# Optimization experiments

Measured on AMD Instinct MI355X. Metric: run time of the kernel, lower is better.

Reference implementation:

```python
import jax, jax.numpy as jnp
import numpy as np

N = 35709   # vertices
F = 70789   # triangles
B = 64
CAMERA_DISTANCE = 10.0
FOCAL = 1015.0
IMAGE_SIZE = 224

SH_A = (np.pi, 2 * np.pi / np.sqrt(3.0), 2 * np.pi / np.sqrt(8.0))
SH_C = (1 / np.sqrt(4 * np.pi), np.sqrt(3.0) / np.sqrt(4 * np.pi), 3 * np.sqrt(5.0) / np.sqrt(12 * np.pi))


def _persc_proj():
    center = IMAGE_SIZE / 2
    m = np.array([FOCAL, 0, center, 0, FOCAL, center, 0, 0, 1], dtype=np.float32).reshape(3, 3).T
    return jnp.asarray(m)


def setup_inputs() -> dict:
    key = jax.random.key(0)
    ks = jax.random.split(key, 9)
    return {
        "coeffs": jax.random.normal(ks[0], (B, 257), jnp.float32),
        "meanshape": jax.random.normal(ks[1], (3 * N,), jnp.float32),
        "idBase": jax.random.normal(ks[2], (3 * N, 80), jnp.float32),
        "exBase": jax.random.normal(ks[3], (3 * N, 64), jnp.float32),
        "meantex": jax.random.uniform(ks[4], (3 * N,), jnp.float32) * 255.0,
        "texBase": jax.random.normal(ks[5], (3 * N, 80), jnp.float32),
        "persc_proj": _persc_proj(),
        "init_lit": jnp.array([0.8, 0, 0, 0, 0, 0, 0, 0, 0], jnp.float32).reshape(1, 1, 9),
        "point_buf": jax.random.randint(ks[6], (N, 8), 0, F + 1),   # index F = zero-pad row
        "face_buf": jax.random.randint(ks[7], (F, 3), 0, N),
        "keypoints": jax.random.randint(ks[8], (68,), 0, N),
    }


def _l2norm(x):
    # matches torch F.normalize(p=2, eps=1e-12)
    return x / jnp.maximum(jnp.linalg.norm(x, axis=-1, keepdims=True), 1e-12)


def _rotation(angles):
    x, y, z = angles[:, 0], angles[:, 1], angles[:, 2]
    o, zr = jnp.ones_like(x), jnp.zeros_like(x)
    cx, sx = jnp.cos(x), jnp.sin(x)
    cy, sy = jnp.cos(y), jnp.sin(y)
    cz, sz = jnp.cos(z), jnp.sin(z)
    rx = jnp.stack([o, zr, zr, zr, cx, -sx, zr, sx, cx], -1).reshape(-1, 3, 3)
    ry = jnp.stack([cy, zr, sy, zr, o, zr, -sy, zr, cy], -1).reshape(-1, 3, 3)
    rz = jnp.stack([cz, -sz, zr, sz, cz, zr, zr, zr, o], -1).reshape(-1, 3, 3)
    return jnp.transpose(rz @ ry @ rx, (0, 2, 1))


def _compute_norm(face_shape, face_buf, point_buf):
    tri = face_shape[:, face_buf]                 # (B, F, 3verts, 3xyz) gather
    e1 = tri[:, :, 0] - tri[:, :, 1]
    e2 = tri[:, :, 1] - tri[:, :, 2]
    fn = _l2norm(jnp.cross(e1, e2))               # (B, F, 3)
    fn = jnp.concatenate([fn, jnp.zeros((fn.shape[0], 1, 3), fn.dtype)], axis=1)
    vn = jnp.sum(fn[:, point_buf], axis=2)        # (B, N, 3) gather-sum over 8 faces
    return _l2norm(vn)


def _compute_color(face_texture, face_norm, gamma, init_lit):
    a, c = SH_A, SH_C
    g = gamma.reshape(gamma.shape[0], 3, 9) + init_lit   # (B, 3, 9)
    g = jnp.transpose(g, (0, 2, 1))                      # (B, 9, 3)
    nx, ny, nz = face_norm[..., 0:1], face_norm[..., 1:2], face_norm[..., 2:3]
    Y = jnp.concatenate([
        a[0] * c[0] * jnp.ones_like(nx),
        -a[1] * c[1] * ny,
        a[1] * c[1] * nz,
        -a[1] * c[1] * nx,
        a[2] * c[2] * nx * ny,
        -a[2] * c[2] * ny * nz,
        0.5 * a[2] * c[2] / np.sqrt(3.0) * (3 * nz ** 2 - 1),
        -a[2] * c[2] * nx * nz,
        0.5 * a[2] * c[2] * (nx ** 2 - ny ** 2)], axis=-1)   # (B, N, 9)
    rgb = jnp.einsum('bnk,bkc->bnc', Y, g)
    return rgb * face_texture


def reference(coeffs, meanshape, idBase, exBase, meantex, texBase, persc_proj, init_lit, point_buf, face_buf, keypoints):
    id_c, ex_c, tex_c = coeffs[:, 0:80], coeffs[:, 80:144], coeffs[:, 144:224]
    angles, gamma, trans = coeffs[:, 224:227], coeffs[:, 227:254], coeffs[:, 254:257]
    Bsz = coeffs.shape[0]
    # shape blending (dense GEMMs)
    shape_flat = (jnp.einsum('ij,aj->ai', idBase, id_c)
                  + jnp.einsum('ij,aj->ai', exBase, ex_c)
                  + meanshape[None])
    face_shape = shape_flat.reshape(Bsz, -1, 3)
    rot = _rotation(angles)
    face_shape_t = face_shape @ rot + trans[:, None, :]
    # to camera: z -> camera_distance - z
    face_vertex = jnp.concatenate([face_shape_t[..., :2], CAMERA_DISTANCE - face_shape_t[..., 2:]], axis=-1)
    # perspective projection
    proj = face_vertex @ persc_proj
    face_proj = proj[..., :2] / proj[..., 2:]
    landmark = face_proj[:, keypoints, :]
    # texture blending
    face_texture = ((jnp.einsum('ij,aj->ai', texBase, tex_c) + meantex[None]) / 255.0).reshape(Bsz, -1, 3)
    # mesh normals on untransformed shape, rotated into camera frame
    face_norm = _compute_norm(face_shape, face_buf, point_buf)
    face_norm_r = face_norm @ rot
    face_color = _compute_color(face_texture, face_norm_r, gamma, init_lit)
    return face_vertex, face_color, landmark
```

## Files before the change

kernel.cpp:

```cpp
#include <hip/hip_runtime.h>

#define N_V 35709
#define N_F 70789
#define NR  (3*N_V)
#define NB  64

#define WS_ROT    0
#define WS_GM     576
#define WS_CTRS   2304
#define WS_CTRT   11520
#define WS_SHAPET 16640

__global__ __launch_bounds__(64) void k_setup_rot(
    const float* __restrict__ coeffs, const float* __restrict__ init_lit,
    float* __restrict__ rotM, float* __restrict__ gm)
{
    int b = threadIdx.x;
    const float* cb = coeffs + b * 257;

    float ax = cb[224], ay = cb[225], az = cb[226];
    float cx = cosf(ax), sx = sinf(ax);
    float cy = cosf(ay), sy = sinf(ay);
    float cz = cosf(az), sz = sinf(az);
    float m[9];
    m[0] = cz * cy;
    m[1] = cz * sy * sx - sz * cx;
    m[2] = sz * sx + cz * sy * cx;
    m[3] = sz * cy;
    m[4] = cz * cx + sz * sy * sx;
    m[5] = sz * sy * cx - cz * sx;
    m[6] = -sy;
    m[7] = cy * sx;
    m[8] = cy * cx;
#pragma unroll
    for (int k = 0; k < 9; k++) rotM[b * 9 + k] = m[k];

#pragma unroll
    for (int k = 0; k < 9; k++) {
        float il = init_lit[k];
#pragma unroll
        for (int c = 0; c < 3; c++)
            gm[b * 27 + k * 3 + c] = cb[227 + c * 9 + k] + il;
    }
}

__global__ __launch_bounds__(64) void k_transpose(
    const float* __restrict__ coeffs,
    float* __restrict__ ctrS, float* __restrict__ ctrT)
{
    int j = blockIdx.x;
    int b = threadIdx.x;
    float v = coeffs[b * 257 + j];
    if (j < 144) ctrS[j * 64 + b] = v;
    else         ctrT[(j - 144) * 64 + b] = v;
}

__global__ __launch_bounds__(256) void k_gemm_tile(
    const float* __restrict__ idBase, const float* __restrict__ exBase,
    const float* __restrict__ texBase, const float* __restrict__ meanshape,
    const float* __restrict__ meantex,
    const float* __restrict__ ctrS, const float* __restrict__ ctrT,
    float* __restrict__ shapeT,
    float* __restrict__ texT,
    float* __restrict__ shape3,
    int write_s3, int tex_transposed)
{
    __shared__ __align__(16) float As[16][68];
    __shared__ __align__(16) float Bs[16][64];

    const int t  = threadIdx.x;
    const int tn = t & 15;
    const int tm = t >> 4;
    const int r0 = blockIdx.x * 64;

    const int srow = t >> 2;
    const int sc   = t & 3;
    int srg = r0 + srow; if (srg > NR - 1) srg = NR - 1;

    float acc[4][4];

#pragma unroll
    for (int i = 0; i < 4; i++)
#pragma unroll
        for (int j = 0; j < 4; j++) acc[i][j] = 0.f;

    for (int kc = 0; kc < 9; kc++) {
        const float* src;
        int ld, k0;
        if (kc < 5) { src = idBase; ld = 80; k0 = kc * 16; }
        else        { src = exBase; ld = 64; k0 = (kc - 5) * 16; }

        {
            float4 v = *(const float4*)(src + (size_t)srg * ld + k0 + sc * 4);
            As[sc * 4 + 0][srow] = v.x;
            As[sc * 4 + 1][srow] = v.y;
            As[sc * 4 + 2][srow] = v.z;
            As[sc * 4 + 3][srow] = v.w;
        }
        ((float4*)&Bs[0][0])[t] = ((const float4*)(ctrS + (size_t)kc * 16 * 64))[t];
        __syncthreads();

#pragma unroll
        for (int k = 0; k < 16; k++) {
            float4 a = *(const float4*)&As[k][tm * 4];
            float4 b = *(const float4*)&Bs[k][tn * 4];
            float av[4] = {a.x, a.y, a.z, a.w};
            float bv[4] = {b.x, b.y, b.z, b.w};
#pragma unroll
            for (int i = 0; i < 4; i++)
#pragma unroll
                for (int j = 0; j < 4; j++)
                    acc[i][j] += av[i] * bv[j];
        }
        __syncthreads();
    }

#pragma unroll
    for (int i = 0; i < 4; i++) {
        int rg = r0 + tm * 4 + i;
        if (rg < NR) {
            float ms = meanshape[rg];
            float s0 = acc[i][0] + ms, s1 = acc[i][1] + ms;
            float s2 = acc[i][2] + ms, s3 = acc[i][3] + ms;
            float4 o = {s0, s1, s2, s3};
            *(float4*)(shapeT + (size_t)rg * 64 + tn * 4) = o;
            if (write_s3) {
                int v = rg / 3;
                int c = rg - v * 3;
                float* p = shape3 + ((size_t)v * 64 + tn * 4) * 3 + c;
                p[0] = s0; p[3] = s1; p[6] = s2; p[9] = s3;
            }
        }
    }

#pragma unroll
    for (int i = 0; i < 4; i++)
#pragma unroll
        for (int j = 0; j < 4; j++) acc[i][j] = 0.f;

    for (int kc = 0; kc < 5; kc++) {
        int k0 = kc * 16;
        {
            float4 v = *(const float4*)(texBase + (size_t)srg * 80 + k0 + sc * 4);
            As[sc * 4 + 0][srow] = v.x;
            As[sc * 4 + 1][srow] = v.y;
            As[sc * 4 + 2][srow] = v.z;
            As[sc * 4 + 3][srow] = v.w;
        }
        ((float4*)&Bs[0][0])[t] = ((const float4*)(ctrT + (size_t)kc * 16 * 64))[t];
        __syncthreads();

#pragma unroll
        for (int k = 0; k < 16; k++) {
            float4 a = *(const float4*)&As[k][tm * 4];
            float4 b = *(const float4*)&Bs[k][tn * 4];
            float av[4] = {a.x, a.y, a.z, a.w};
            float bv[4] = {b.x, b.y, b.z, b.w};
#pragma unroll
            for (int i = 0; i < 4; i++)
#pragma unroll
                for (int j = 0; j < 4; j++)
                    acc[i][j] += av[i] * bv[j];
        }
        __syncthreads();
    }

    const float inv255 = 1.0f / 255.0f;
    if (tex_transposed) {
#pragma unroll
        for (int i = 0; i < 4; i++) {
            int rg = r0 + tm * 4 + i;
            if (rg < NR) {
                float mt = meantex[rg];
                float4 o = {(acc[i][0] + mt) * inv255, (acc[i][1] + mt) * inv255,
                            (acc[i][2] + mt) * inv255, (acc[i][3] + mt) * inv255};
                *(float4*)(texT + (size_t)rg * 64 + tn * 4) = o;
            }
        }
    } else {
#pragma unroll
        for (int i = 0; i < 4; i++) {
            int rg = r0 + tm * 4 + i;
            if (rg < NR) {
                float mt = meantex[rg];
#pragma unroll
                for (int j = 0; j < 4; j++)
                    texT[(size_t)(tn * 4 + j) * NR + rg] = (acc[i][j] + mt) * inv255;
            }
        }
    }
}

__global__ __launch_bounds__(256) void k_facenorm3(
    const float* __restrict__ shape3,
    const int* __restrict__ face_buf,
    float* __restrict__ fnT3)
{
    int wave = threadIdx.x >> 6;
    int b    = threadIdx.x & 63;
    int f0   = blockIdx.x * 32 + wave * 8;
#pragma unroll
    for (int fr = 0; fr < 8; fr++) {
        int f = f0 + fr;
        if (f < N_F) {
            int i0 = face_buf[f * 3 + 0];
            int i1 = face_buf[f * 3 + 1];
            int i2 = face_buf[f * 3 + 2];
            const float* p0 = shape3 + ((size_t)i0 * 64 + b) * 3;
            const float* p1 = shape3 + ((size_t)i1 * 64 + b) * 3;
            const float* p2 = shape3 + ((size_t)i2 * 64 + b) * 3;
            float p0x = p0[0], p0y = p0[1], p0z = p0[2];
            float p1x = p1[0], p1y = p1[1], p1z = p1[2];
            float p2x = p2[0], p2y = p2[1], p2z = p2[2];
            float e1x = p0x - p1x, e1y = p0y - p1y, e1z = p0z - p1z;
            float e2x = p1x - p2x, e2y = p1y - p2y, e2z = p1z - p2z;
            float ccx = e1y * e2z - e1z * e2y;
            float ccy = e1z * e2x - e1x * e2z;
            float ccz = e1x * e2y - e1y * e2x;
            float l = sqrtf(ccx * ccx + ccy * ccy + ccz * ccz);
            float inv = 1.0f / fmaxf(l, 1e-12f);
            float* o = fnT3 + ((size_t)f * 64 + b) * 3;
            o[0] = ccx * inv; o[1] = ccy * inv; o[2] = ccz * inv;
        } else if (f == N_F) {
            float* o = fnT3 + ((size_t)f * 64 + b) * 3;
            o[0] = 0.f; o[1] = 0.f; o[2] = 0.f;
        }
    }
}

__global__ __launch_bounds__(256) void k_facenorm(
    const float* __restrict__ shapeT,
    const int* __restrict__ face_buf,
    float* __restrict__ fnT3)
{
    int wave = threadIdx.x >> 6;
    int b    = threadIdx.x & 63;
    int f0   = blockIdx.x * 32 + wave * 8;
#pragma unroll
    for (int fr = 0; fr < 8; fr++) {
        int f = f0 + fr;
        if (f < N_F) {
            int i0 = face_buf[f * 3 + 0];
            int i1 = face_buf[f * 3 + 1];
            int i2 = face_buf[f * 3 + 2];
            float p0x = shapeT[(size_t)(3 * i0)     * 64 + b];
            float p0y = shapeT[(size_t)(3 * i0 + 1) * 64 + b];
            float p0z = shapeT[(size_t)(3 * i0 + 2) * 64 + b];
            float p1x = shapeT[(size_t)(3 * i1)     * 64 + b];
            float p1y = shapeT[(size_t)(3 * i1 + 1) * 64 + b];
            float p1z = shapeT[(size_t)(3 * i1 + 2) * 64 + b];
            float p2x = shapeT[(size_t)(3 * i2)     * 64 + b];
            float p2y = shapeT[(size_t)(3 * i2 + 1) * 64 + b];
            float p2z = shapeT[(size_t)(3 * i2 + 2) * 64 + b];
            float e1x = p0x - p1x, e1y = p0y - p1y, e1z = p0z - p1z;
            float e2x = p1x - p2x, e2y = p1y - p2y, e2z = p1z - p2z;
            float ccx = e1y * e2z - e1z * e2y;
            float ccy = e1z * e2x - e1x * e2z;
            float ccz = e1x * e2y - e1y * e2x;
            float l = sqrtf(ccx * ccx + ccy * ccy + ccz * ccz);
            float inv = 1.0f / fmaxf(l, 1e-12f);
            float* o = fnT3 + ((size_t)f * 64 + b) * 3;
            o[0] = ccx * inv; o[1] = ccy * inv; o[2] = ccz * inv;
        } else if (f == N_F) {
            float* o = fnT3 + ((size_t)f * 64 + b) * 3;
            o[0] = 0.f; o[1] = 0.f; o[2] = 0.f;
        }
    }
}

__global__ __launch_bounds__(256) void k_vertex_fn(
    const float* __restrict__ shapeT,
    const float* __restrict__ texT,
    const float* __restrict__ fnT3,
    const float* __restrict__ rotM, const float* __restrict__ gm,
    const float* __restrict__ coeffs,
    const int* __restrict__ point_buf,
    float* __restrict__ out_vertex, float* __restrict__ out_color)
{
    __shared__ float sh[64 * 49];
    int wave = threadIdx.x >> 6;
    int b    = threadIdx.x & 63;
    int v0   = blockIdx.x * 16;
    int nvalid = N_V - v0; if (nvalid > 16) nvalid = 16;
    int kmax = 3 * nvalid;

    float m0 = rotM[b * 9 + 0], m1 = rotM[b * 9 + 1], m2 = rotM[b * 9 + 2];
    float m3 = rotM[b * 9 + 3], m4 = rotM[b * 9 + 4], m5 = rotM[b * 9 + 5];
    float m6 = rotM[b * 9 + 6], m7 = rotM[b * 9 + 7], m8 = rotM[b * 9 + 8];
    float tx = coeffs[b * 257 + 254], ty = coeffs[b * 257 + 255], tz = coeffs[b * 257 + 256];
    float g[27];
#pragma unroll
    for (int k = 0; k < 27; k++) g[k] = gm[b * 27 + k];

    const float A0C0 = 0.8862269254527580f;
    const float A1C1 = 1.7724538509055159f;
    const float A2C2 = 2.4270323912f;
    const float C6   = 0.7006239022f;
    const float C8   = 1.2135161956f;

    int pf[4][8];
    float sxv[4], syv[4], szv[4];
    float t0v[4], t1v[4], t2v[4];
#pragma unroll
    for (int vr = 0; vr < 4; vr++) {
        int v = v0 + wave * 4 + vr;
        int vc = (v < N_V) ? v : (N_V - 1);
#pragma unroll
        for (int k = 0; k < 8; k++) pf[vr][k] = point_buf[vc * 8 + k];
        sxv[vr] = shapeT[(size_t)(3 * vc)     * 64 + b];
        syv[vr] = shapeT[(size_t)(3 * vc + 1) * 64 + b];
        szv[vr] = shapeT[(size_t)(3 * vc + 2) * 64 + b];
        t0v[vr] = texT[(size_t)(3 * vc)     * 64 + b];
        t1v[vr] = texT[(size_t)(3 * vc + 1) * 64 + b];
        t2v[vr] = texT[(size_t)(3 * vc + 2) * 64 + b];
    }

    float vert[4][3];
    float col[4][3];

#pragma unroll
    for (int vr = 0; vr < 4; vr++) {
        float fx[8], fy[8], fz[8];
#pragma unroll
        for (int k = 0; k < 8; k++) {
            const float* fp = fnT3 + ((size_t)pf[vr][k] * 64 + b) * 3;
            fx[k] = fp[0]; fy[k] = fp[1]; fz[k] = fp[2];
        }

        float vx = m0 * sxv[vr] + m1 * syv[vr] + m2 * szv[vr] + tx;
        float vy = m3 * sxv[vr] + m4 * syv[vr] + m5 * szv[vr] + ty;
        float vz = m6 * sxv[vr] + m7 * syv[vr] + m8 * szv[vr] + tz;
        vert[vr][0] = vx; vert[vr][1] = vy; vert[vr][2] = 10.0f - vz;

        float nx = 0.f, ny = 0.f, nz = 0.f;
#pragma unroll
        for (int k = 0; k < 8; k++) { nx += fx[k]; ny += fy[k]; nz += fz[k]; }
        float l = sqrtf(nx * nx + ny * ny + nz * nz);
        float inv = 1.0f / fmaxf(l, 1e-12f);
        nx *= inv; ny *= inv; nz *= inv;

        float rx = m0 * nx + m1 * ny + m2 * nz;
        float ry = m3 * nx + m4 * ny + m5 * nz;
        float rz = m6 * nx + m7 * ny + m8 * nz;

        float Y0 = A0C0;
        float Y1 = -A1C1 * ry;
        float Y2 =  A1C1 * rz;
        float Y3 = -A1C1 * rx;
        float Y4 =  A2C2 * rx * ry;
        float Y5 = -A2C2 * ry * rz;
        float Y6 =  C6 * (3.f * rz * rz - 1.f);
        float Y7 = -A2C2 * rx * rz;
        float Y8 =  C8 * (rx * rx - ry * ry);

        float tex3[3] = {t0v[vr], t1v[vr], t2v[vr]};
#pragma unroll
        for (int c = 0; c < 3; c++) {
            float rgb = Y0 * g[0 + c] + Y1 * g[3 + c] + Y2 * g[6 + c] + Y3 * g[9 + c] +
                        Y4 * g[12 + c] + Y5 * g[15 + c] + Y6 * g[18 + c] + Y7 * g[21 + c] +
                        Y8 * g[24 + c];
            col[vr][c] = rgb * tex3[c];
        }
    }

#pragma unroll
    for (int vr = 0; vr < 4; vr++)
#pragma unroll
        for (int c = 0; c < 3; c++)
            sh[b * 49 + (wave * 4 + vr) * 3 + c] = vert[vr][c];
    __syncthreads();
#pragma unroll 4
    for (int it = 0; it < 12; it++) {
        int f = it * 256 + threadIdx.x;
        int bb = f / 48, k = f - bb * 48;
        if (k < kmax)
            __builtin_nontemporal_store(sh[bb * 49 + k],
                                        out_vertex + (size_t)bb * NR + 3 * (size_t)v0 + k);
    }
    __syncthreads();

#pragma unroll
    for (int vr = 0; vr < 4; vr++)
#pragma unroll
        for (int c = 0; c < 3; c++)
            sh[b * 49 + (wave * 4 + vr) * 3 + c] = col[vr][c];
    __syncthreads();
#pragma unroll 4
    for (int it = 0; it < 12; it++) {
        int f = it * 256 + threadIdx.x;
        int bb = f / 48, k = f - bb * 48;
        if (k < kmax)
            __builtin_nontemporal_store(sh[bb * 49 + k],
                                        out_color + (size_t)bb * NR + 3 * (size_t)v0 + k);
    }
}

__global__ __launch_bounds__(256) void k_vertex(
    const float* __restrict__ shapeT,
    const float* __restrict__ texT,
    const float* __restrict__ rotM, const float* __restrict__ gm,
    const float* __restrict__ coeffs,
    const int* __restrict__ point_buf, const int* __restrict__ face_buf,
    float* __restrict__ out_vertex, float* __restrict__ out_color,
    int tex_in_out)
{
    __shared__ float sh[64 * 97];
    int wave = threadIdx.x >> 6;
    int b    = threadIdx.x & 63;
    int v0   = blockIdx.x * 32;
    int nvalid = N_V - v0; if (nvalid > 32) nvalid = 32;
    int kmax = 3 * nvalid;

    float m0 = rotM[b * 9 + 0], m1 = rotM[b * 9 + 1], m2 = rotM[b * 9 + 2];
    float m3 = rotM[b * 9 + 3], m4 = rotM[b * 9 + 4], m5 = rotM[b * 9 + 5];
    float m6 = rotM[b * 9 + 6], m7 = rotM[b * 9 + 7], m8 = rotM[b * 9 + 8];
    float tx = coeffs[b * 257 + 254], ty = coeffs[b * 257 + 255], tz = coeffs[b * 257 + 256];
    float g[27];
#pragma unroll
    for (int k = 0; k < 27; k++) g[k] = gm[b * 27 + k];

    const float A0C0 = 0.8862269254527580f;
    const float A1C1 = 1.7724538509055159f;
    const float A2C2 = 2.4270323912f;
    const float C6   = 0.7006239022f;
    const float C8   = 1.2135161956f;

    float vert[8][3];
    float col[8][3];

#pragma unroll
    for (int vr = 0; vr < 8; vr++) {
        int v = v0 + wave * 8 + vr;
        bool valid = (v < N_V);
        int vc = valid ? v : (N_V - 1);

        float sx0 = shapeT[(size_t)(3 * vc)     * 64 + b];
        float sy0 = shapeT[(size_t)(3 * vc + 1) * 64 + b];
        float sz0 = shapeT[(size_t)(3 * vc + 2) * 64 + b];

        float vx = m0 * sx0 + m1 * sy0 + m2 * sz0 + tx;
        float vy = m3 * sx0 + m4 * sy0 + m5 * sz0 + ty;
        float vz = m6 * sx0 + m7 * sy0 + m8 * sz0 + tz;
        vert[vr][0] = vx; vert[vr][1] = vy; vert[vr][2] = 10.0f - vz;

        float nx = 0.f, ny = 0.f, nz = 0.f;
#pragma unroll
        for (int k = 0; k < 8; k++) {
            int f = point_buf[vc * 8 + k];
            if (f < N_F) {
                int i0 = face_buf[f * 3], i1 = face_buf[f * 3 + 1], i2 = face_buf[f * 3 + 2];
                float p0x = shapeT[(size_t)(3 * i0)     * 64 + b];
                float p0y = shapeT[(size_t)(3 * i0 + 1) * 64 + b];
                float p0z = shapeT[(size_t)(3 * i0 + 2) * 64 + b];
                float p1x = shapeT[(size_t)(3 * i1)     * 64 + b];
                float p1y = shapeT[(size_t)(3 * i1 + 1) * 64 + b];
                float p1z = shapeT[(size_t)(3 * i1 + 2) * 64 + b];
                float p2x = shapeT[(size_t)(3 * i2)     * 64 + b];
                float p2y = shapeT[(size_t)(3 * i2 + 1) * 64 + b];
                float p2z = shapeT[(size_t)(3 * i2 + 2) * 64 + b];
                float e1x = p0x - p1x, e1y = p0y - p1y, e1z = p0z - p1z;
                float e2x = p1x - p2x, e2y = p1y - p2y, e2z = p1z - p2z;
                float ccx = e1y * e2z - e1z * e2y;
                float ccy = e1z * e2x - e1x * e2z;
                float ccz = e1x * e2y - e1y * e2x;
                float l = sqrtf(ccx * ccx + ccy * ccy + ccz * ccz);
                float inv = 1.0f / fmaxf(l, 1e-12f);
                nx += ccx * inv; ny += ccy * inv; nz += ccz * inv;
            }
        }
        float l = sqrtf(nx * nx + ny * ny + nz * nz);
        float inv = 1.0f / fmaxf(l, 1e-12f);
        nx *= inv; ny *= inv; nz *= inv;

        float rx = m0 * nx + m1 * ny + m2 * nz;
        float ry = m3 * nx + m4 * ny + m5 * nz;
        float rz = m6 * nx + m7 * ny + m8 * nz;

        float Y0 = A0C0;
        float Y1 = -A1C1 * ry;
        float Y2 =  A1C1 * rz;
        float Y3 = -A1C1 * rx;
        float Y4 =  A2C2 * rx * ry;
        float Y5 = -A2C2 * ry * rz;
        float Y6 =  C6 * (3.f * rz * rz - 1.f);
        float Y7 = -A2C2 * rx * rz;
        float Y8 =  C8 * (rx * rx - ry * ry);

        float t0, t1, t2;
        if (tex_in_out) {
            size_t ob = (size_t)b * NR + 3 * (size_t)vc;
            t0 = out_color[ob]; t1 = out_color[ob + 1]; t2 = out_color[ob + 2];
        } else {
            t0 = texT[(size_t)(3 * vc)     * 64 + b];
            t1 = texT[(size_t)(3 * vc + 1) * 64 + b];
            t2 = texT[(size_t)(3 * vc + 2) * 64 + b];
        }
        float tex3[3] = {t0, t1, t2};
#pragma unroll
        for (int c = 0; c < 3; c++) {
            float rgb = Y0 * g[0 + c] + Y1 * g[3 + c] + Y2 * g[6 + c] + Y3 * g[9 + c] +
                        Y4 * g[12 + c] + Y5 * g[15 + c] + Y6 * g[18 + c] + Y7 * g[21 + c] +
                        Y8 * g[24 + c];
            col[vr][c] = rgb * tex3[c];
        }
    }

#pragma unroll
    for (int vr = 0; vr < 8; vr++)
#pragma unroll
        for (int c = 0; c < 3; c++)
            sh[b * 97 + (wave * 8 + vr) * 3 + c] = vert[vr][c];
    __syncthreads();
#pragma unroll 4
    for (int it = 0; it < 24; it++) {
        int f = it * 256 + threadIdx.x;
        int bb = f / 96, k = f - bb * 96;
        if (k < kmax)
            __builtin_nontemporal_store(sh[bb * 97 + k],
                                        out_vertex + (size_t)bb * NR + 3 * (size_t)v0 + k);
    }
    __syncthreads();

#pragma unroll
    for (int vr = 0; vr < 8; vr++)
#pragma unroll
        for (int c = 0; c < 3; c++)
            sh[b * 97 + (wave * 8 + vr) * 3 + c] = col[vr][c];
    __syncthreads();
#pragma unroll 4
    for (int it = 0; it < 24; it++) {
        int f = it * 256 + threadIdx.x;
        int bb = f / 96, k = f - bb * 96;
        if (k < kmax)
            __builtin_nontemporal_store(sh[bb * 97 + k],
                                        out_color + (size_t)bb * NR + 3 * (size_t)v0 + k);
    }
}

__global__ __launch_bounds__(64) void k_landmark(
    const float* __restrict__ shapeT, const int* __restrict__ keypoints,
    const float* __restrict__ rotM, const float* __restrict__ coeffs,
    const float* __restrict__ P,
    float* __restrict__ out_lm)
{
    int l = blockIdx.x;
    int b = threadIdx.x;
    int kp = keypoints[l];

    float m0 = rotM[b * 9 + 0], m1 = rotM[b * 9 + 1], m2 = rotM[b * 9 + 2];
    float m3 = rotM[b * 9 + 3], m4 = rotM[b * 9 + 4], m5 = rotM[b * 9 + 5];
    float m6 = rotM[b * 9 + 6], m7 = rotM[b * 9 + 7], m8 = rotM[b * 9 + 8];
    float tx = coeffs[b * 257 + 254], ty = coeffs[b * 257 + 255], tz = coeffs[b * 257 + 256];

    float sx0 = shapeT[(size_t)(3 * kp)     * 64 + b];
    float sy0 = shapeT[(size_t)(3 * kp + 1) * 64 + b];
    float sz0 = shapeT[(size_t)(3 * kp + 2) * 64 + b];

    float x = m0 * sx0 + m1 * sy0 + m2 * sz0 + tx;
    float y = m3 * sx0 + m4 * sy0 + m5 * sz0 + ty;
    float z = 10.0f - (m6 * sx0 + m7 * sy0 + m8 * sz0 + tz);

    float p0 = x * P[0] + y * P[3] + z * P[6];
    float p1 = x * P[1] + y * P[4] + z * P[7];
    float p2 = x * P[2] + y * P[5] + z * P[8];

    size_t o = ((size_t)b * 68 + l) * 2;
    out_lm[o]     = p0 / p2;
    out_lm[o + 1] = p1 / p2;
}

extern "C" void kernel_launch(void* const* d_in, const int* in_sizes, int n_in,
                              void* d_out, int out_size, void* d_ws, size_t ws_size,
                              hipStream_t stream) {
    const float* coeffs    = (const float*)d_in[0];
    const float* meanshape = (const float*)d_in[1];
    const float* idBase    = (const float*)d_in[2];
    const float* exBase    = (const float*)d_in[3];
    const float* meantex   = (const float*)d_in[4];
    const float* texBase   = (const float*)d_in[5];
    const float* persc     = (const float*)d_in[6];
    const float* init_lit  = (const float*)d_in[7];
    const int*   point_buf = (const int*)d_in[8];
    const int*   face_buf  = (const int*)d_in[9];
    const int*   keypoints = (const int*)d_in[10];

    float* ws = (float*)d_ws;
    float* rotM = ws + WS_ROT;
    float* gm   = ws + WS_GM;
    float* ctrS = ws + WS_CTRS;
    float* ctrT = ws + WS_CTRT;
    float* shapeT = ws + WS_SHAPET;

    float* out_vertex = (float*)d_out;
    float* out_color  = out_vertex + (size_t)NB * NR;
    float* out_lm     = out_color  + (size_t)NB * NR;

    size_t NRx64   = (size_t)NR * 64;
    size_t fn3_len = (size_t)(N_F + 1) * 64 * 3;
    size_t sh3_len = (size_t)N_V * 64 * 3;

    size_t need_tex = ((size_t)WS_SHAPET + 2 * NRx64) * sizeof(float);
    size_t need_fn  = need_tex + fn3_len * sizeof(float);
    size_t need_s3  = need_fn + sh3_len * sizeof(float);

    int tex_transposed = (ws_size >= need_tex) ? 1 : 0;
    int use_fn         = (ws_size >= need_fn) ? 1 : 0;
    int use_s3         = (ws_size >= need_s3) ? 1 : 0;

    float* texT   = tex_transposed ? (shapeT + NRx64) : out_color;
    float* fnT3   = shapeT + 2 * NRx64;
    float* shape3 = fnT3 + fn3_len;

    k_setup_rot<<<1, 64, 0, stream>>>(coeffs, init_lit, rotM, gm);
    k_transpose<<<224, 64, 0, stream>>>(coeffs, ctrS, ctrT);

    int gb = (NR + 63) / 64;
    k_gemm_tile<<<gb, 256, 0, stream>>>(idBase, exBase, texBase, meanshape,
                                        meantex, ctrS, ctrT, shapeT, texT,
                                        shape3, use_s3, tex_transposed);

    if (use_fn) {
        int fb = (N_F + 1 + 31) / 32;
        if (use_s3) {
            k_facenorm3<<<fb, 256, 0, stream>>>(shape3, face_buf, fnT3);
        } else {
            k_facenorm<<<fb, 256, 0, stream>>>(shapeT, face_buf, fnT3);
        }
        int vb = (N_V + 15) / 16;
        k_vertex_fn<<<vb, 256, 0, stream>>>(shapeT, texT, fnT3, rotM, gm, coeffs,
                                            point_buf, out_vertex, out_color);
    } else {
        int vb = (N_V + 31) / 32;
        k_vertex<<<vb, 256, 0, stream>>>(shapeT, tex_transposed ? texT : nullptr,
                                         rotM, gm, coeffs, point_buf, face_buf,
                                         out_vertex, out_color,
                                         tex_transposed ? 0 : 1);
    }

    k_landmark<<<68, 64, 0, stream>>>(shapeT, keypoints, rotM, coeffs, persc, out_lm);
}
```

Baseline: 285.4 us.

## Write only packed shape layout via shared-memory staged coalesced epilogue

When the packed vertex-major shape buffer is enabled, the GEMM epilogue stops writing the row-major shapeT copy and writes only shape3. It stages each half-tile through shared memory so the scattered stride-3 stores become contiguous, coalesced writes. The vertex and landmark kernels gain a flag to read shape from the packed layout, removing one full shape write pass. The cost is extra syncthreads, integer division in the store loop, and reuse of the GEMM shared buffer for staging.

```diff
diff --git a/kernel.cpp b/kernel.cpp
--- a/kernel.cpp
+++ b/kernel.cpp
@@ -65,8 +65,10 @@
     float* __restrict__ shape3,
     int write_s3, int tex_transposed)
 {
-    __shared__ __align__(16) float As[16][68];
-    __shared__ __align__(16) float Bs[16][64];
+    __shared__ __align__(16) float smem[2112];
+    float (*As)[68] = (float (*)[68])smem;
+    float (*Bs)[64] = (float (*)[64])(smem + 1088);
+    float* epi = smem;
 
     const int t  = threadIdx.x;
     const int tn = t & 15;
@@ -115,20 +117,53 @@
         __syncthreads();
     }
 
+    float msv[4];
 #pragma unroll
     for (int i = 0; i < 4; i++) {
         int rg = r0 + tm * 4 + i;
-        if (rg < NR) {
-            float ms = meanshape[rg];
-            float s0 = acc[i][0] + ms, s1 = acc[i][1] + ms;
-            float s2 = acc[i][2] + ms, s3 = acc[i][3] + ms;
-            float4 o = {s0, s1, s2, s3};
-            *(float4*)(shapeT + (size_t)rg * 64 + tn * 4) = o;
-            if (write_s3) {
-                int v = rg / 3;
-                int c = rg - v * 3;
-                float* p = shape3 + ((size_t)v * 64 + tn * 4) * 3 + c;
-                p[0] = s0; p[3] = s1; p[6] = s2; p[9] = s3;
+        msv[i] = meanshape[(rg < NR) ? rg : (NR - 1)];
+    }
+
+    if (write_s3) {
+#pragma unroll
+        for (int h = 0; h < 2; h++) {
+            if ((tm >> 3) == h) {
+                int lr0 = (tm & 7) * 4;
+#pragma unroll
+                for (int i = 0; i < 4; i++)
+#pragma unroll
+                    for (int j = 0; j < 4; j++)
+                        epi[(lr0 + i) * 65 + tn * 4 + j] = acc[i][j] + msv[i];
+            }
+            __syncthreads();
+            int R0   = r0 + h * 32;
+            int Rend = R0 + 32; if (Rend > NR) Rend = NR;
+            if (R0 < NR) {
+                int vlo  = R0 / 3;
+                int vhi  = (Rend - 1) / 3;
+                int base = vlo * 192;
+                int span = (vhi + 1) * 192 - base;
+                for (int q = t; q < span; q += 256) {
+                    int addr = base + q;
+                    int v    = addr / 192;
+                    int rem  = addr - v * 192;
+                    int b    = rem / 3;
+                    int c    = rem - b * 3;
+                    int r    = 3 * v + c;
+                    if (r >= R0 && r < Rend)
+                        shape3[addr] = epi[(r - R0) * 65 + b];
+                }
+            }
+            __syncthreads();
+        }
+    } else {
+#pragma unroll
+        for (int i = 0; i < 4; i++) {
+            int rg = r0 + tm * 4 + i;
+            if (rg < NR) {
+                float4 o = {acc[i][0] + msv[i], acc[i][1] + msv[i],
+                            acc[i][2] + msv[i], acc[i][3] + msv[i]};
+                *(float4*)(shapeT + (size_t)rg * 64 + tn * 4) = o;
             }
         }
     }
@@ -269,13 +304,14 @@
 }
 
 __global__ __launch_bounds__(256) void k_vertex_fn(
-    const float* __restrict__ shapeT,
+    const float* __restrict__ shp,
     const float* __restrict__ texT,
     const float* __restrict__ fnT3,
     const float* __restrict__ rotM, const float* __restrict__ gm,
     const float* __restrict__ coeffs,
     const int* __restrict__ point_buf,
-    float* __restrict__ out_vertex, float* __restrict__ out_color)
+    float* __restrict__ out_vertex, float* __restrict__ out_color,
+    int packed)
 {
     __shared__ float sh[64 * 49];
     int wave = threadIdx.x >> 6;
@@ -307,9 +343,14 @@
         int vc = (v < N_V) ? v : (N_V - 1);
 #pragma unroll
         for (int k = 0; k < 8; k++) pf[vr][k] = point_buf[vc * 8 + k];
-        sxv[vr] = shapeT[(size_t)(3 * vc)     * 64 + b];
-        syv[vr] = shapeT[(size_t)(3 * vc + 1) * 64 + b];
-        szv[vr] = shapeT[(size_t)(3 * vc + 2) * 64 + b];
+        if (packed) {
+            const float* sp = shp + ((size_t)vc * 64 + b) * 3;
+            sxv[vr] = sp[0]; syv[vr] = sp[1]; szv[vr] = sp[2];
+        } else {
+            sxv[vr] = shp[(size_t)(3 * vc)     * 64 + b];
+            syv[vr] = shp[(size_t)(3 * vc + 1) * 64 + b];
+            szv[vr] = shp[(size_t)(3 * vc + 2) * 64 + b];
+        }
         t0v[vr] = texT[(size_t)(3 * vc)     * 64 + b];
         t1v[vr] = texT[(size_t)(3 * vc + 1) * 64 + b];
         t2v[vr] = texT[(size_t)(3 * vc + 2) * 64 + b];
@@ -538,10 +579,10 @@
 }
 
 __global__ __launch_bounds__(64) void k_landmark(
-    const float* __restrict__ shapeT, const int* __restrict__ keypoints,
+    const float* __restrict__ shp, const int* __restrict__ keypoints,
     const float* __restrict__ rotM, const float* __restrict__ coeffs,
     const float* __restrict__ P,
-    float* __restrict__ out_lm)
+    float* __restrict__ out_lm, int packed)
 {
     int l = blockIdx.x;
     int b = threadIdx.x;
@@ -552,9 +593,15 @@
     float m6 = rotM[b * 9 + 6], m7 = rotM[b * 9 + 7], m8 = rotM[b * 9 + 8];
     float tx = coeffs[b * 257 + 254], ty = coeffs[b * 257 + 255], tz = coeffs[b * 257 + 256];
 
-    float sx0 = shapeT[(size_t)(3 * kp)     * 64 + b];
-    float sy0 = shapeT[(size_t)(3 * kp + 1) * 64 + b];
-    float sz0 = shapeT[(size_t)(3 * kp + 2) * 64 + b];
+    float sx0, sy0, sz0;
+    if (packed) {
+        const float* sp = shp + ((size_t)kp * 64 + b) * 3;
+        sx0 = sp[0]; sy0 = sp[1]; sz0 = sp[2];
+    } else {
+        sx0 = shp[(size_t)(3 * kp)     * 64 + b];
+        sy0 = shp[(size_t)(3 * kp + 1) * 64 + b];
+        sz0 = shp[(size_t)(3 * kp + 2) * 64 + b];
+    }
 
     float x = m0 * sx0 + m1 * sy0 + m2 * sz0 + tx;
     float y = m3 * sx0 + m4 * sy0 + m5 * sz0 + ty;
@@ -623,19 +670,26 @@
         int fb = (N_F + 1 + 31) / 32;
         if (use_s3) {
             k_facenorm3<<<fb, 256, 0, stream>>>(shape3, face_buf, fnT3);
+            int vb = (N_V + 15) / 16;
+            k_vertex_fn<<<vb, 256, 0, stream>>>(shape3, texT, fnT3, rotM, gm, coeffs,
+                                                point_buf, out_vertex, out_color, 1);
+            k_landmark<<<68, 64, 0, stream>>>(shape3, keypoints, rotM, coeffs, persc,
+                                              out_lm, 1);
         } else {
             k_facenorm<<<fb, 256, 0, stream>>>(shapeT, face_buf, fnT3);
-        }
-        int vb = (N_V + 15) / 16;
-        k_vertex_fn<<<vb, 256, 0, stream>>>(shapeT, texT, fnT3, rotM, gm, coeffs,
-                                            point_buf, out_vertex, out_color);
+            int vb = (N_V + 15) / 16;
+            k_vertex_fn<<<vb, 256, 0, stream>>>(shapeT, texT, fnT3, rotM, gm, coeffs,
+                                                point_buf, out_vertex, out_color, 0);
+            k_landmark<<<68, 64, 0, stream>>>(shapeT, keypoints, rotM, coeffs, persc,
+                                              out_lm, 0);
+        }
     } else {
         int vb = (N_V + 31) / 32;
         k_vertex<<<vb, 256, 0, stream>>>(shapeT, tex_transposed ? texT : nullptr,
                                          rotM, gm, coeffs, point_buf, face_buf,
                                          out_vertex, out_color,
                                          tex_transposed ? 0 : 1);
-    }
-
-    k_landmark<<<68, 64, 0, stream>>>(shapeT, keypoints, rotM, coeffs, persc, out_lm);
-}
+        k_landmark<<<68, 64, 0, stream>>>(shapeT, keypoints, rotM, coeffs, persc,
+                                          out_lm, 0);
+    }
+}
```

Result: faster. 278.5 us (-2.4%).
